# Optimization experiments

Measured on AMD Instinct MI355X. Metric: run time of the kernel, lower is better.

Reference implementation:

```python
import jax, jax.numpy as jnp
import numpy as np

B, S, D, E, H = 4, 2048, 1024, 8, 4096

def setup_inputs() -> dict:
    key = jax.random.key(0)
    ks = jax.random.split(key, 7)
    scale_d = 1.0 / np.sqrt(D)
    scale_h = 1.0 / np.sqrt(H)
    return {
        "x": jax.random.normal(ks[0], (B, S, D), dtype=jnp.float32),
        "Wr": jax.random.uniform(ks[1], (D, E), jnp.float32, -scale_d, scale_d),
        "br": jnp.zeros((E,), jnp.float32),
        "W1": jax.random.uniform(ks[2], (E, D, H), jnp.float32, -scale_d, scale_d),
        "b1": jax.random.uniform(ks[3], (E, H), jnp.float32, -scale_d, scale_d),
        "W2": jax.random.uniform(ks[4], (E, H, D), jnp.float32, -scale_h, scale_h),
        "b2": jax.random.uniform(ks[5], (E, D), jnp.float32, -scale_h, scale_h),
    }

def reference(x, Wr, br, W1, b1, W2, b2):
    # Router: softmax then argmax (top-1). Note: original does NOT scale
    # expert output by the routing weight and never applies capacity drop.
    route_logits = jnp.einsum("bsd,de->bse", x, Wr) + br
    routing_weights = jax.nn.softmax(route_logits, axis=-1)
    selected_expert = jnp.argmax(routing_weights, axis=-1)  # [B, S] int

    num_experts = W1.shape[0]
    out = jnp.zeros_like(x)
    # Fixed small loop over experts (structurally distinct weight slices);
    # select-by-mask keeps shapes static under jit.
    for e in range(num_experts):
        h = jax.nn.gelu(jnp.einsum("bsd,dh->bsh", x, W1[e]) + b1[e], approximate=False)
        y = jnp.einsum("bsh,hd->bsd", h, W2[e]) + b2[e]
        out = jnp.where((selected_expert == e)[..., None], y, out)
    return out
```

## Files before the change

### kernel.cpp

```cpp
#include <hip/hip_runtime.h>
#include <math.h>

#define TOK   8192
#define DD    1024
#define EE    8
#define HH    4096
#define MAXROWS 10240
#define MAXMT 40

typedef unsigned short u16;
typedef unsigned int   u32;
typedef __bf16 bf16x8 __attribute__((ext_vector_type(8)));
typedef float  f32x4  __attribute__((ext_vector_type(4)));

__device__ __forceinline__ u16 f2bf(float f) {
  union { float f; u32 u; } v; v.f = f;
  u32 r = v.u + 0x7fffu + ((v.u >> 16) & 1u);
  return (u16)(r >> 16);
}

__device__ __forceinline__ void gload16(const void* g, void* l) {
  __builtin_amdgcn_global_load_lds(
      (const __attribute__((address_space(1))) void*)g,
      (__attribute__((address_space(3))) void*)l, 16, 0, 0);
}

__global__ void k_init(int* rowmap, int* counts, int* fill) {
  int i = blockIdx.x * 256 + threadIdx.x;
  if (i < MAXROWS) rowmap[i] = -1;
  if (blockIdx.x == 0 && threadIdx.x < EE) { counts[threadIdx.x] = 0; fill[threadIdx.x] = 0; }
}

__global__ __launch_bounds__(256)
void k_route(const float* __restrict__ x, const float* __restrict__ Wr,
             const float* __restrict__ br, int* __restrict__ eid,
             int* __restrict__ counts, u16* __restrict__ xb) {
  int t = blockIdx.x * 4 + (threadIdx.x >> 6);
  int lt = threadIdx.x & 63;
  const float4* xr = (const float4*)(x + (size_t)t * DD);
  u16* xbr = xb + (size_t)t * DD;
  const float4* wrp = (const float4*)Wr;
  float acc[EE];
  #pragma unroll
  for (int e = 0; e < EE; ++e) acc[e] = 0.f;
  #pragma unroll
  for (int i = 0; i < 4; ++i) {
    int d4 = lt + 64 * i;
    float4 v = xr[d4];
    u32 p0 = (u32)f2bf(v.x) | ((u32)f2bf(v.y) << 16);
    u32 p1 = (u32)f2bf(v.z) | ((u32)f2bf(v.w) << 16);
    ((uint2*)xbr)[d4] = make_uint2(p0, p1);
    float vv[4] = { v.x, v.y, v.z, v.w };
    #pragma unroll
    for (int dd = 0; dd < 4; ++dd) {
      float xv = vv[dd];
      float4 a = wrp[(size_t)(d4 * 4 + dd) * 2];
      float4 b = wrp[(size_t)(d4 * 4 + dd) * 2 + 1];
      acc[0] += xv * a.x; acc[1] += xv * a.y; acc[2] += xv * a.z; acc[3] += xv * a.w;
      acc[4] += xv * b.x; acc[5] += xv * b.y; acc[6] += xv * b.z; acc[7] += xv * b.w;
    }
  }
  #pragma unroll
  for (int e = 0; e < EE; ++e)
    #pragma unroll
    for (int off = 32; off > 0; off >>= 1) acc[e] += __shfl_down(acc[e], off);
  if (lt == 0) {
    float best = -1e30f; int be = 0;
    #pragma unroll
    for (int e = 0; e < EE; ++e) {
      float v = acc[e] + br[e];
      if (v > best) { best = v; be = e; }
    }
    eid[t] = be;
    atomicAdd(&counts[be], 1);
  }
}

__global__ void k_scan(const int* __restrict__ counts, int* __restrict__ poff) {
  if (threadIdx.x == 0) {
    int off = 0; poff[0] = 0;
    for (int e = 0; e < EE; ++e) { off += ((counts[e] + 255) >> 8) << 8; poff[e + 1] = off; }
  }
}

__global__ void k_fillmap(const int* __restrict__ eid, const int* __restrict__ poff,
                          int* __restrict__ fill, int* __restrict__ rowmap) {
  int t = blockIdx.x * 256 + threadIdx.x;
  if (t < TOK) {
    int e = eid[t];
    int pos = atomicAdd(&fill[e], 1);
    rowmap[poff[e] + pos] = t;
  }
}

__global__ __launch_bounds__(256)
void k_transpose(const float* __restrict__ W, u16* __restrict__ WT, int K, int N) {
  __shared__ float tile[64][33];
  const int e = blockIdx.z;
  const int n0 = blockIdx.x * 32, k0 = blockIdx.y * 64;
  const float* We = W + (size_t)e * K * N;
  u16* WTe = WT + (size_t)e * K * N;
  const int t = threadIdx.x;
  const int kk = t >> 3, nn = (t & 7) * 4;
  #pragma unroll
  for (int i = 0; i < 2; ++i) {
    const float4 v = *(const float4*)&We[(size_t)(k0 + kk + 32 * i) * N + n0 + nn];
    tile[kk + 32 * i][nn]     = v.x;
    tile[kk + 32 * i][nn + 1] = v.y;
    tile[kk + 32 * i][nn + 2] = v.z;
    tile[kk + 32 * i][nn + 3] = v.w;
  }
  __syncthreads();
  const int n = t >> 3, c = t & 7;
  u32 p[4];
  #pragma unroll
  for (int j = 0; j < 4; ++j) {
    u32 lo = f2bf(tile[c * 8 + 2 * j][n]);
    u32 hi = f2bf(tile[c * 8 + 2 * j + 1][n]);
    p[j] = lo | (hi << 16);
  }
  *(uint4*)&WTe[(size_t)(n0 + n) * K + k0 + c * 8] = make_uint4(p[0], p[1], p[2], p[3]);
}

template <int KDIM, int NDIM, bool G2>
__global__ __launch_bounds__(512, 2)
void k_gemm(const u16* __restrict__ Abase, const u16* __restrict__ WT,
            const float* __restrict__ bias, const int* __restrict__ poff,
            const int* __restrict__ rowmap, u16* __restrict__ hout,
            float* __restrict__ yout) {
  extern __shared__ char lds[];
  const int mt = blockIdx.y;
  const int mbase = mt * 256;
  if (mbase >= poff[EE]) return;
  int e = 0;
  #pragma unroll
  for (int q = 1; q < EE; ++q) e += (mbase >= poff[q]) ? 1 : 0;

  const int nbase = blockIdx.x * 256;
  const int tid = threadIdx.x;
  const int lt = tid & 63;
  const int wid = tid >> 6;
  const int wr = wid >> 2, wc = wid & 3;

  const int row0 = tid >> 2;
  const int cl = (tid & 3) ^ ((tid >> 3) & 3);
  int r0, r1;
  if (G2) { r0 = mbase + row0; r1 = r0 + 128; }
  else {
    r0 = rowmap[mbase + row0];       if (r0 < 0) r0 = 0;
    r1 = rowmap[mbase + 128 + row0]; if (r1 < 0) r1 = 0;
  }
  const u16* gA0 = Abase + (size_t)r0 * KDIM + cl * 8;
  const u16* gA1 = Abase + (size_t)r1 * KDIM + cl * 8;
  const u16* wte = WT + (size_t)e * NDIM * KDIM + (size_t)nbase * KDIM;
  const u16* gB0 = wte + (size_t)row0 * KDIM + cl * 8;
  const u16* gB1 = wte + (size_t)(128 + row0) * KDIM + cl * 8;

  char* dA = lds + tid * 16;
  char* dB = lds + 65536 + tid * 16;

#define STAGE(B, T) do {                               \
    const int ko = (T) * 32;                           \
    gload16(gA0 + ko, dA + (B) * 16384);               \
    gload16(gA1 + ko, dA + (B) * 16384 + 8192);        \
    gload16(gB0 + ko, dB + (B) * 16384);               \
    gload16(gB1 + ko, dB + (B) * 16384 + 8192);        \
  } while (0)

  const int cph = ((lt >> 4) ^ ((lt >> 1) & 3)) << 4;
  const char* pA = lds + (wr * 128 + (lt & 15)) * 64 + cph;
  const char* pB = lds + 65536 + (wc * 64 + (lt & 15)) * 64 + cph;

  f32x4 acc[8][4] = {};

#define GSTEP(T, B, WAITI, DOSTAGE) do {                                              \
    asm volatile("s_waitcnt vmcnt(" WAITI ")\n\ts_barrier" ::: "memory");             \
    if (DOSTAGE) STAGE(((B) + 3) & 3, (T) + 3);                                       \
    bf16x8 af[8], bg[4];                                                              \
    _Pragma("unroll")                                                                 \
    for (int m = 0; m < 8; ++m) af[m] = *(const bf16x8*)(pA + (B) * 16384 + m * 1024);\
    _Pragma("unroll")                                                                 \
    for (int n = 0; n < 4; ++n) bg[n] = *(const bf16x8*)(pB + (B) * 16384 + n * 1024);\
    __builtin_amdgcn_s_setprio(1);                                                    \
    _Pragma("unroll")                                                                 \
    for (int m = 0; m < 8; ++m)                                                       \
      _Pragma("unroll")                                                               \
      for (int n = 0; n < 4; ++n)                                                     \
        acc[m][n] = __builtin_amdgcn_mfma_f32_16x16x32_bf16(af[m], bg[n], acc[m][n], 0, 0, 0); \
    __builtin_amdgcn_s_setprio(0);                                                    \
  } while (0)

  STAGE(0, 0); STAGE(1, 1); STAGE(2, 2);
  const int KT = KDIM / 32;
  #pragma unroll 1
  for (int kt = 0; kt < KT - 4; kt += 4) {
    GSTEP(kt + 0, 0, "8", true);
    GSTEP(kt + 1, 1, "8", true);
    GSTEP(kt + 2, 2, "8", true);
    GSTEP(kt + 3, 3, "8", true);
  }
  GSTEP(KT - 4, 0, "8", true);
  GSTEP(KT - 3, 1, "8", false);
  GSTEP(KT - 2, 2, "4", false);
  GSTEP(KT - 1, 3, "0", false);
#undef GSTEP
#undef STAGE

  const int cl16 = lt & 15, rq = (lt >> 4) * 4;
  float bv[4];
  #pragma unroll
  for (int n = 0; n < 4; ++n)
    bv[n] = bias[(size_t)e * NDIM + nbase + wc * 64 + n * 16 + cl16];

  const int colb = nbase + wc * 64 + cl16;
  #pragma unroll
  for (int m = 0; m < 8; ++m) {
    const int rb = mbase + wr * 128 + m * 16 + rq;
    #pragma unroll
    for (int r = 0; r < 4; ++r) {
      const int grow = rb + r;
      if (G2) {
        const int tok = rowmap[grow];
        if (tok >= 0) {
          float* yp = yout + (size_t)tok * NDIM + colb;
          #pragma unroll
          for (int n = 0; n < 4; ++n) yp[n * 16] = acc[m][n][r] + bv[n];
        }
      } else {
        u16* hp = hout + (size_t)grow * NDIM + colb;
        #pragma unroll
        for (int n = 0; n < 4; ++n) {
          float v = acc[m][n][r] + bv[n];
          v = 0.5f * v * (1.0f + erff(v * 0.70710678118654752f));
          hp[n * 16] = f2bf(v);
        }
      }
    }
  }
}

extern "C" void kernel_launch(void* const* d_in, const int* in_sizes, int n_in,
                              void* d_out, int out_size, void* d_ws, size_t ws_size,
                              hipStream_t stream) {
  const float* x  = (const float*)d_in[0];
  const float* Wr = (const float*)d_in[1];
  const float* br = (const float*)d_in[2];
  const float* W1 = (const float*)d_in[3];
  const float* b1 = (const float*)d_in[4];
  const float* W2 = (const float*)d_in[5];
  const float* b2 = (const float*)d_in[6];
  float* out = (float*)d_out;

  char* ws = (char*)d_ws;
  int* eid    = (int*)(ws + 0);
  int* counts = (int*)(ws + 32768);
  int* fill   = (int*)(ws + 32832);
  int* poff   = (int*)(ws + 32896);
  int* rowmap = (int*)(ws + 33024);
  u16* xbf    = (u16*)(ws + 73984);
  u16* w1t    = (u16*)(ws + 16851200);
  u16* w2t    = (u16*)(ws + 83960064);
  u16* hbuf   = (u16*)(ws + 151068928);

  hipFuncSetAttribute((const void*)k_gemm<DD, HH, false>,
                      hipFuncAttributeMaxDynamicSharedMemorySize, 131072);
  hipFuncSetAttribute((const void*)k_gemm<HH, DD, true>,
                      hipFuncAttributeMaxDynamicSharedMemorySize, 131072);

  k_init<<<MAXROWS / 256, 256, 0, stream>>>(rowmap, counts, fill);
  k_route<<<TOK / 4, 256, 0, stream>>>(x, Wr, br, eid, counts, xbf);
  k_scan<<<1, 64, 0, stream>>>(counts, poff);
  k_fillmap<<<TOK / 256, 256, 0, stream>>>(eid, poff, fill, rowmap);
  k_transpose<<<dim3(HH / 32, DD / 64, EE), 256, 0, stream>>>(W1, w1t, DD, HH);
  k_transpose<<<dim3(DD / 32, HH / 64, EE), 256, 0, stream>>>(W2, w2t, HH, DD);
  k_gemm<DD, HH, false><<<dim3(HH / 256, MAXMT), 512, 131072, stream>>>(xbf, w1t, b1, poff, rowmap, hbuf, nullptr);
  k_gemm<HH, DD, true><<<dim3(DD / 256, MAXMT), 512, 131072, stream>>>(hbuf, w2t, b2, poff, rowmap, nullptr, out);
}
```

Before: 692.1 us.

## Split GEMM LDS reads for overlap, remap workgroups for XCDs, fuse small kernels

The GEMM main loop is restructured so each K-step reads the B fragments and half of the A fragments before the barrier, then reads the second half of A while the first half's MFMAs issue. The next step's first-half read is prefetched after the barrier. This aims to hide LDS latency behind matrix work, using one barrier per step. Workgroup IDs are remapped in an XCD-aware pattern to improve L2 locality, the two weight-transpose launches are merged into one, and the rowmap init is folded into the router kernel to cut launch overhead. The reordered LDS reads depend on the barrier placement protecting buffer reuse across the 4-slot ring.

```diff
diff --git a/kernel.cpp b/kernel.cpp
--- a/kernel.cpp
+++ b/kernel.cpp
@@ -25,16 +25,19 @@
       (__attribute__((address_space(3))) void*)l, 16, 0, 0);
 }
 
-__global__ void k_init(int* rowmap, int* counts, int* fill) {
-  int i = blockIdx.x * 256 + threadIdx.x;
-  if (i < MAXROWS) rowmap[i] = -1;
-  if (blockIdx.x == 0 && threadIdx.x < EE) { counts[threadIdx.x] = 0; fill[threadIdx.x] = 0; }
+__global__ void k_init(int* counts, int* fill) {
+  if (threadIdx.x < EE) { counts[threadIdx.x] = 0; fill[threadIdx.x] = 0; }
 }
 
 __global__ __launch_bounds__(256)
 void k_route(const float* __restrict__ x, const float* __restrict__ Wr,
              const float* __restrict__ br, int* __restrict__ eid,
-             int* __restrict__ counts, u16* __restrict__ xb) {
+             int* __restrict__ counts, u16* __restrict__ xb,
+             int* __restrict__ rowmap) {
+  if (threadIdx.x < 5) {
+    int ri = blockIdx.x * 5 + threadIdx.x;
+    if (ri < MAXROWS) rowmap[ri] = -1;
+  }
   int t = blockIdx.x * 4 + (threadIdx.x >> 6);
   int lt = threadIdx.x & 63;
   const float4* xr = (const float4*)(x + (size_t)t * DD);
@@ -76,10 +79,13 @@
   }
 }
 
-__global__ void k_scan(const int* __restrict__ counts, int* __restrict__ poff) {
+__global__ void k_scan(const int* __restrict__ counts, int* __restrict__ poff,
+                       int* __restrict__ fill) {
   if (threadIdx.x == 0) {
     int off = 0; poff[0] = 0;
-    for (int e = 0; e < EE; ++e) { off += ((counts[e] + 255) >> 8) << 8; poff[e + 1] = off; }
+    for (int e = 0; e < EE; ++e) {
+      off += ((counts[e] + 255) >> 8) << 8; poff[e + 1] = off; fill[e] = 0;
+    }
   }
 }
 
@@ -94,10 +100,17 @@
 }
 
 __global__ __launch_bounds__(256)
-void k_transpose(const float* __restrict__ W, u16* __restrict__ WT, int K, int N) {
+void k_transpose2(const float* __restrict__ W1, u16* __restrict__ W1T,
+                  const float* __restrict__ W2, u16* __restrict__ W2T) {
   __shared__ float tile[64][33];
-  const int e = blockIdx.z;
-  const int n0 = blockIdx.x * 32, k0 = blockIdx.y * 64;
+  int b = blockIdx.x;
+  const float* W; u16* WT; int K, N, nx;
+  if (b < (HH / 32) * (DD / 64) * EE) { W = W1; WT = W1T; K = DD; N = HH; nx = HH / 32; }
+  else { b -= (HH / 32) * (DD / 64) * EE; W = W2; WT = W2T; K = HH; N = DD; nx = DD / 32; }
+  const int nk = K / 64;
+  const int e = b / (nx * nk);
+  const int r = b % (nx * nk);
+  const int n0 = (r % nx) * 32, k0 = (r / nx) * 64;
   const float* We = W + (size_t)e * K * N;
   u16* WTe = WT + (size_t)e * K * N;
   const int t = threadIdx.x;
@@ -129,14 +142,18 @@
             const int* __restrict__ rowmap, u16* __restrict__ hout,
             float* __restrict__ yout) {
   extern __shared__ char lds[];
-  const int mt = blockIdx.y;
+  constexpr int NT = NDIM / 256;
+  constexpr int NWG = NT * MAXMT;
+  int bid = blockIdx.y * NT + blockIdx.x;
+  bid = (bid & 7) * (NWG / 8) + (bid >> 3);
+  const int mt = bid / NT;
+  const int nbase = (bid % NT) * 256;
   const int mbase = mt * 256;
   if (mbase >= poff[EE]) return;
   int e = 0;
   #pragma unroll
   for (int q = 1; q < EE; ++q) e += (mbase >= poff[q]) ? 1 : 0;
 
-  const int nbase = blockIdx.x * 256;
   const int tid = threadIdx.x;
   const int lt = tid & 63;
   const int wid = tid >> 6;
@@ -156,55 +173,77 @@
   const u16* gB0 = wte + (size_t)row0 * KDIM + cl * 8;
   const u16* gB1 = wte + (size_t)(128 + row0) * KDIM + cl * 8;
 
-  char* dA = lds + tid * 16;
-  char* dB = lds + 65536 + tid * 16;
-
-#define STAGE(B, T) do {                               \
-    const int ko = (T) * 32;                           \
-    gload16(gA0 + ko, dA + (B) * 16384);               \
-    gload16(gA1 + ko, dA + (B) * 16384 + 8192);        \
-    gload16(gB0 + ko, dB + (B) * 16384);               \
-    gload16(gB1 + ko, dB + (B) * 16384 + 8192);        \
-  } while (0)
+  char* sA = lds + tid * 16;
+  char* sB = lds + 65536 + tid * 16;
 
   const int cph = ((lt >> 4) ^ ((lt >> 1) & 3)) << 4;
   const char* pA = lds + (wr * 128 + (lt & 15)) * 64 + cph;
   const char* pB = lds + 65536 + (wc * 64 + (lt & 15)) * 64 + cph;
 
   f32x4 acc[8][4] = {};
-
-#define GSTEP(T, B, WAITI, DOSTAGE) do {                                              \
-    asm volatile("s_waitcnt vmcnt(" WAITI ")\n\ts_barrier" ::: "memory");             \
-    if (DOSTAGE) STAGE(((B) + 3) & 3, (T) + 3);                                       \
-    bf16x8 af[8], bg[4];                                                              \
-    _Pragma("unroll")                                                                 \
-    for (int m = 0; m < 8; ++m) af[m] = *(const bf16x8*)(pA + (B) * 16384 + m * 1024);\
-    _Pragma("unroll")                                                                 \
-    for (int n = 0; n < 4; ++n) bg[n] = *(const bf16x8*)(pB + (B) * 16384 + n * 1024);\
-    __builtin_amdgcn_s_setprio(1);                                                    \
-    _Pragma("unroll")                                                                 \
-    for (int m = 0; m < 8; ++m)                                                       \
-      _Pragma("unroll")                                                               \
-      for (int n = 0; n < 4; ++n)                                                     \
-        acc[m][n] = __builtin_amdgcn_mfma_f32_16x16x32_bf16(af[m], bg[n], acc[m][n], 0, 0, 0); \
-    __builtin_amdgcn_s_setprio(0);                                                    \
+  bf16x8 af0[4], af1[4], bg[4];
+
+#define STG(slot) do {                                            \
+    const int sb_ = ((slot) & 3) * 16384;                         \
+    const int ko_ = (slot) * 32;                                  \
+    gload16(gA0 + ko_, sA + sb_);                                 \
+    gload16(gA1 + ko_, sA + sb_ + 8192);                          \
+    gload16(gB0 + ko_, sB + sb_);                                 \
+    gload16(gB1 + ko_, sB + sb_ + 8192);                          \
   } while (0)
 
-  STAGE(0, 0); STAGE(1, 1); STAGE(2, 2);
-  const int KT = KDIM / 32;
+#define RD0(slot) do {                                            \
+    const int sb_ = ((slot) & 3) * 16384;                         \
+    _Pragma("unroll")                                             \
+    for (int n = 0; n < 4; ++n) bg[n]  = *(const bf16x8*)(pB + sb_ + n * 1024); \
+    _Pragma("unroll")                                             \
+    for (int m = 0; m < 4; ++m) af0[m] = *(const bf16x8*)(pA + sb_ + m * 1024); \
+  } while (0)
+
+#define RD1(slot) do {                                            \
+    const int sb_ = ((slot) & 3) * 16384;                         \
+    _Pragma("unroll")                                             \
+    for (int m = 0; m < 4; ++m) af1[m] = *(const bf16x8*)(pA + sb_ + 4096 + m * 1024); \
+  } while (0)
+
+#define MM(AF, mo) do {                                           \
+    __builtin_amdgcn_s_setprio(1);                                \
+    _Pragma("unroll")                                             \
+    for (int m = 0; m < 4; ++m)                                   \
+      _Pragma("unroll")                                           \
+      for (int n = 0; n < 4; ++n)                                 \
+        acc[(mo) + m][n] = __builtin_amdgcn_mfma_f32_16x16x32_bf16( \
+            AF[m], bg[n], acc[(mo) + m][n], 0, 0, 0);             \
+    __builtin_amdgcn_s_setprio(0);                                \
+  } while (0)
+
+  constexpr int NS = KDIM / 32;
+
+  STG(0); STG(1); STG(2);
+  asm volatile("s_waitcnt vmcnt(8)\n\ts_barrier" ::: "memory");
+  RD0(0);
+
   #pragma unroll 1
-  for (int kt = 0; kt < KT - 4; kt += 4) {
-    GSTEP(kt + 0, 0, "8", true);
-    GSTEP(kt + 1, 1, "8", true);
-    GSTEP(kt + 2, 2, "8", true);
-    GSTEP(kt + 3, 3, "8", true);
-  }
-  GSTEP(KT - 4, 0, "8", true);
-  GSTEP(KT - 3, 1, "8", false);
-  GSTEP(KT - 2, 2, "4", false);
-  GSTEP(KT - 1, 3, "0", false);
-#undef GSTEP
-#undef STAGE
+  for (int s = 0; s < NS - 3; ++s) {
+    STG(s + 3);
+    RD1(s);
+    MM(af0, 0);
+    MM(af1, 4);
+    asm volatile("s_waitcnt vmcnt(8)\n\ts_barrier" ::: "memory");
+    RD0(s + 1);
+  }
+  RD1(NS - 3); MM(af0, 0); MM(af1, 4);
+  asm volatile("s_waitcnt vmcnt(4)\n\ts_barrier" ::: "memory");
+  RD0(NS - 2);
+  RD1(NS - 2); MM(af0, 0); MM(af1, 4);
+  asm volatile("s_waitcnt vmcnt(0)\n\ts_barrier" ::: "memory");
+  RD0(NS - 1);
+  RD1(NS - 1); MM(af0, 0); MM(af1, 4);
+
+#undef MM
+#undef RD1
+#undef RD0
+#undef STG
 
   const int cl16 = lt & 15, rq = (lt >> 4) * 4;
   float bv[4];
@@ -267,12 +306,11 @@
   hipFuncSetAttribute((const void*)k_gemm<HH, DD, true>,
                       hipFuncAttributeMaxDynamicSharedMemorySize, 131072);
 
-  k_init<<<MAXROWS / 256, 256, 0, stream>>>(rowmap, counts, fill);
-  k_route<<<TOK / 4, 256, 0, stream>>>(x, Wr, br, eid, counts, xbf);
-  k_scan<<<1, 64, 0, stream>>>(counts, poff);
+  k_init<<<1, 64, 0, stream>>>(counts, fill);
+  k_route<<<TOK / 4, 256, 0, stream>>>(x, Wr, br, eid, counts, xbf, rowmap);
+  k_scan<<<1, 64, 0, stream>>>(counts, poff, fill);
   k_fillmap<<<TOK / 256, 256, 0, stream>>>(eid, poff, fill, rowmap);
-  k_transpose<<<dim3(HH / 32, DD / 64, EE), 256, 0, stream>>>(W1, w1t, DD, HH);
-  k_transpose<<<dim3(DD / 32, HH / 64, EE), 256, 0, stream>>>(W2, w2t, HH, DD);
+  k_transpose2<<<2 * (HH / 32) * (DD / 64) * EE, 256, 0, stream>>>(W1, w1t, W2, w2t);
   k_gemm<DD, HH, false><<<dim3(HH / 256, MAXMT), 512, 131072, stream>>>(xbf, w1t, b1, poff, rowmap, hbuf, nullptr);
   k_gemm<HH, DD, true><<<dim3(DD / 256, MAXMT), 512, 131072, stream>>>(hbuf, w2t, b2, poff, rowmap, nullptr, out);
 }
```

New measurement: 712.6 us. 1.03x slower.
